# Performance work log

Hardware: AMD Instinct MI355X
Metric: run time of the kernel (lower is better)

The kernel has to match this reference:

```python
import jax, jax.numpy as jnp
import numpy as np

DIM = 2048
NUM_HEADS = 16
HEAD_DIM = DIM // NUM_HEADS
ROPE_BASE = 10000.0


def _rope_cache(seq_len):
    inv_freq = 1.0 / (ROPE_BASE ** (jnp.arange(0, HEAD_DIM, 2, dtype=jnp.float32) / HEAD_DIM))
    t = jnp.arange(seq_len, dtype=jnp.float32)
    freqs = jnp.einsum('i,j->ij', t, inv_freq)          # [S, HEAD_DIM//2]
    emb = jnp.concatenate([freqs, freqs], axis=-1)       # [S, HEAD_DIM]
    return jnp.cos(emb), jnp.sin(emb)


def _rotate_half(x):
    x1, x2 = jnp.split(x, 2, axis=-1)
    return jnp.concatenate([-x2, x1], axis=-1)


def setup_inputs() -> dict:
    key = jax.random.key(0)
    kx, kq, ko = jax.random.split(key, 3)
    B, S = 2, 2048
    x = jax.random.normal(kx, (B, S, DIM), dtype=jnp.float32)
    # torch nn.Linear(dim, 3*dim) weight has shape [3*dim, dim]; y = x @ W.T
    w_qkv = jax.random.normal(kq, (3 * DIM, DIM), dtype=jnp.float32) * (DIM ** -0.5)
    w_out = jax.random.normal(ko, (DIM, DIM), dtype=jnp.float32) * (DIM ** -0.5)
    return {"x": x, "w_qkv": w_qkv, "w_out": w_out}


def reference(x, w_qkv, w_out):
    B, S, _ = x.shape
    qkv = x @ w_qkv.T                                   # [B, S, 3*DIM]
    q, k, v = jnp.split(qkv, 3, axis=-1)
    def to_heads(t):
        return t.reshape(B, S, NUM_HEADS, HEAD_DIM).transpose(0, 2, 1, 3)  # [B, H, S, d]
    q, k, v = to_heads(q), to_heads(k), to_heads(v)

    cos, sin = _rope_cache(S)                           # [S, d]
    cos = cos[None, None, :, :]
    sin = sin[None, None, :, :]
    q = q * cos + _rotate_half(q) * sin
    k = k * cos + _rotate_half(k) * sin

    scale = HEAD_DIM ** -0.5
    scores = jnp.einsum('bhqd,bhkd->bhqk', q, k) * scale  # [B, H, S, S]
    causal = jnp.tril(jnp.ones((S, S), dtype=bool))
    scores = jnp.where(causal[None, None], scores, -jnp.inf)
    attn = jax.nn.softmax(scores, axis=-1)
    out = jnp.einsum('bhqk,bhkd->bhqd', attn, v)          # [B, H, S, d]
    out = out.transpose(0, 2, 1, 3).reshape(B, S, DIM)
    return out @ w_out.T
```

## Files before the change

kernel.cpp:

```cpp
#include <hip/hip_runtime.h>
#include <cstdint>
#include <cstddef>

#define NHEADS 16
#define HDIM   128
#define BATCH  2
#define SEQ    2048
#define DMODEL 2048
#define MTOT   (BATCH*SEQ)
#define NQKV   (3*DMODEL)

typedef __attribute__((ext_vector_type(8))) __bf16 bf16x8;
typedef __attribute__((ext_vector_type(4))) float f32x4;
typedef __attribute__((ext_vector_type(8))) unsigned short ushort8v;

__device__ __forceinline__ unsigned short f2bf(float f){
  __bf16 h = (__bf16)f;
  return __builtin_bit_cast(unsigned short, h);
}
__device__ __forceinline__ float bf2f(unsigned short s){
  return __uint_as_float(((uint32_t)s) << 16);
}
__device__ __forceinline__ void gload_lds16(const void* src, void* lds_base){
  __builtin_amdgcn_global_load_lds((const __attribute__((address_space(1))) unsigned int*)src,
                                   (__attribute__((address_space(3))) unsigned int*)lds_base,
                                   16, 0, 0);
}

template<int CTRL>
__device__ __forceinline__ float dppmv(float x){
  return __uint_as_float((unsigned)__builtin_amdgcn_update_dpp(
      0, (int)__float_as_uint(x), CTRL, 0xF, 0xF, true));
}
__device__ __forceinline__ float rmax16(float x){
  x = fmaxf(x, dppmv<0x128>(x));
  x = fmaxf(x, dppmv<0x124>(x));
  x = fmaxf(x, dppmv<0x122>(x));
  x = fmaxf(x, dppmv<0x121>(x));
  return x;
}
__device__ __forceinline__ float rsum16(float x){
  x += dppmv<0x128>(x);
  x += dppmv<0x124>(x);
  x += dppmv<0x122>(x);
  x += dppmv<0x121>(x);
  return x;
}

__global__ void cast3_kernel(const float* __restrict__ s0, unsigned short* __restrict__ d0, int n0,
                             const float* __restrict__ s1, unsigned short* __restrict__ d1, int n1,
                             const float* __restrict__ s2, unsigned short* __restrict__ d2, int n2){
  const int stride = gridDim.x*blockDim.x*8;
  const int base = (blockIdx.x*blockDim.x + threadIdx.x)*8;
  #pragma unroll 1
  for (int a = 0; a < 3; ++a){
    const float* s = a==0 ? s0 : (a==1 ? s1 : s2);
    unsigned short* d = a==0 ? d0 : (a==1 ? d1 : d2);
    const int n = a==0 ? n0 : (a==1 ? n1 : n2);
    for (int i = base; i < n; i += stride){
      float4 x = *reinterpret_cast<const float4*>(s + i);
      float4 y = *reinterpret_cast<const float4*>(s + i + 4);
      ushort8v o;
      o[0]=f2bf(x.x); o[1]=f2bf(x.y); o[2]=f2bf(x.z); o[3]=f2bf(x.w);
      o[4]=f2bf(y.x); o[5]=f2bf(y.y); o[6]=f2bf(y.z); o[7]=f2bf(y.w);
      *reinterpret_cast<ushort8v*>(d + i) = o;
    }
  }
}

template<int MODE>
__global__ __launch_bounds__(512, 2) void gemm2(
    const unsigned short* __restrict__ A,
    const unsigned short* __restrict__ Bw,
    float* __restrict__ Cf,
    unsigned short* __restrict__ qo,
    unsigned short* __restrict__ ko,
    unsigned short* __restrict__ vo,
    int M, int N, int K)
{
  __shared__ __align__(16) unsigned short smem[49152];
  auto lds = reinterpret_cast<unsigned short (*)[3][128*64]>(smem);

  const int lane = threadIdx.x & 63;
  const int wid  = threadIdx.x >> 6;
  const int wm = wid >> 2, wn = wid & 3;
  const int hi = lane >> 4;
  const int l15 = lane & 15;

  const int nwg = gridDim.x * gridDim.y;
  const int bid = blockIdx.y * gridDim.x + blockIdx.x;
  const int swz = (bid & 7) * (nwg >> 3) + (bid >> 3);
  const int by = swz & 31;
  const int bx = swz >> 5;
  const int m0 = by * 128;
  const int n0 = bx * 256;

  const int NT = K >> 6;

  auto stage = [&](const unsigned short* base, int row0, int k0, int buf, int slot){
    const int rlo = wid << 4;
    #pragma unroll
    for (int i=0;i<2;++i){
      const int r = rlo + i*8 + (lane>>3);
      const int csrc = ((lane&7) ^ (lane>>3)) << 3;
      gload_lds16(base + (size_t)(row0 + r)*K + k0 + csrc,
                  &lds[buf][slot][(rlo + i*8)*64]);
    }
  };
  auto frag = [&](const unsigned short* h, int r, int s){
    return *reinterpret_cast<const bf16x8*>(h + r*64 + ((s ^ (r&7)) << 3));
  };

  f32x4 acc[4][4];
  #pragma unroll
  for (int i=0;i<4;++i)
    #pragma unroll
    for (int j=0;j<4;++j) acc[i][j] = (f32x4){0.f,0.f,0.f,0.f};

  stage(A,  m0,      0, 0, 0);
  stage(Bw, n0,      0, 0, 1);
  stage(Bw, n0+128,  0, 0, 2);
  if (NT > 1){
    stage(A, m0, 64, 1, 0);
    asm volatile("s_waitcnt vmcnt(2)" ::: "memory");
  } else {
    asm volatile("s_waitcnt vmcnt(0)" ::: "memory");
  }
  __builtin_amdgcn_sched_barrier(0);
  __builtin_amdgcn_s_barrier();

  bf16x8 Ar[4][2];
  bf16x8 Br[2][2];

  auto tile_body = [&](int kt, int cur){
    const int nxt = cur ^ 1;
    const unsigned short* Ah = &lds[cur][0][0];
    const unsigned short* Bh = &lds[cur][1 + (wn>>1)][0];
    const int rbase = (wn & 1) * 64;

    #pragma unroll
    for (int fm=0;fm<4;++fm)
      #pragma unroll
      for (int kk=0;kk<2;++kk)
        Ar[fm][kk] = frag(Ah, wm*64 + fm*16 + l15, kk*4 + hi);
    #pragma unroll
    for (int nf=0;nf<2;++nf)
      #pragma unroll
      for (int kk=0;kk<2;++kk)
        Br[nf][kk] = frag(Bh, rbase + nf*16 + l15, kk*4 + hi);
    if (kt+1 < NT){
      stage(Bw, n0,     (kt+1)*64, nxt, 1);
      stage(Bw, n0+128, (kt+1)*64, nxt, 2);
    }
    asm volatile("s_waitcnt lgkmcnt(8)" ::: "memory");
    __builtin_amdgcn_sched_barrier(0);
    __builtin_amdgcn_s_barrier();
    asm volatile("s_waitcnt lgkmcnt(0)" ::: "memory");
    __builtin_amdgcn_sched_barrier(0);
    __builtin_amdgcn_s_setprio(1);
    #pragma unroll
    for (int fm=0;fm<4;++fm){
      acc[fm][0] = __builtin_amdgcn_mfma_f32_16x16x32_bf16(Ar[fm][0], Br[0][0], acc[fm][0], 0,0,0);
      acc[fm][0] = __builtin_amdgcn_mfma_f32_16x16x32_bf16(Ar[fm][1], Br[0][1], acc[fm][0], 0,0,0);
      acc[fm][1] = __builtin_amdgcn_mfma_f32_16x16x32_bf16(Ar[fm][0], Br[1][0], acc[fm][1], 0,0,0);
      acc[fm][1] = __builtin_amdgcn_mfma_f32_16x16x32_bf16(Ar[fm][1], Br[1][1], acc[fm][1], 0,0,0);
    }
    __builtin_amdgcn_s_setprio(0);
    __builtin_amdgcn_sched_barrier(0);
    __builtin_amdgcn_s_barrier();

    #pragma unroll
    for (int nf=0;nf<2;++nf)
      #pragma unroll
      for (int kk=0;kk<2;++kk)
        Br[nf][kk] = frag(Bh, rbase + 32 + nf*16 + l15, kk*4 + hi);
    if (kt+2 < NT) stage(A, m0, (kt+2)*64, cur, 0);
    __builtin_amdgcn_sched_barrier(0);
    __builtin_amdgcn_s_barrier();
    asm volatile("s_waitcnt lgkmcnt(0)" ::: "memory");
    __builtin_amdgcn_sched_barrier(0);
    __builtin_amdgcn_s_setprio(1);
    #pragma unroll
    for (int fm=0;fm<4;++fm){
      acc[fm][2] = __builtin_amdgcn_mfma_f32_16x16x32_bf16(Ar[fm][0], Br[0][0], acc[fm][2], 0,0,0);
      acc[fm][2] = __builtin_amdgcn_mfma_f32_16x16x32_bf16(Ar[fm][1], Br[0][1], acc[fm][2], 0,0,0);
      acc[fm][3] = __builtin_amdgcn_mfma_f32_16x16x32_bf16(Ar[fm][0], Br[1][0], acc[fm][3], 0,0,0);
      acc[fm][3] = __builtin_amdgcn_mfma_f32_16x16x32_bf16(Ar[fm][1], Br[1][1], acc[fm][3], 0,0,0);
    }
    __builtin_amdgcn_s_setprio(0);
    if (kt+2 < NT)      asm volatile("s_waitcnt vmcnt(2)" ::: "memory");
    else if (kt+1 < NT) asm volatile("s_waitcnt vmcnt(0)" ::: "memory");
    __builtin_amdgcn_sched_barrier(0);
    __builtin_amdgcn_s_barrier();
  };

  for (int kt2 = 0; kt2 < NT; kt2 += 2){
    tile_body(kt2,     0);
    tile_body(kt2 + 1, 1);
  }

  if (MODE == 0 && (n0 >> 11) == 2){
    __builtin_amdgcn_s_barrier();
    unsigned short* trsp = smem;
    #pragma unroll
    for (int fm=0;fm<4;++fm){
      const int srow = wm*64 + fm*16 + hi*4;
      #pragma unroll
      for (int p=0;p<4;++p){
        const int dcol = wn*64 + p*16 + l15;
        f32x4 v = acc[fm][p];
        ushort4 pk;
        pk.x=f2bf(v[0]); pk.y=f2bf(v[1]); pk.z=f2bf(v[2]); pk.w=f2bf(v[3]);
        *reinterpret_cast<ushort4*>(trsp + dcol*136 + srow) = pk;
      }
    }
    __syncthreads();
    const int bb  = m0 >> 11;
    const int ss0 = m0 & 2047;
    const size_t vrow = (size_t)(bb*2048 + (n0 - 4096));
    const int t = threadIdx.x;
    #pragma unroll
    for (int it=0; it<8; ++it){
      const int dl = it*32 + (t>>4);
      const int ch = t & 15;
      ushort8v val = *reinterpret_cast<const ushort8v*>(trsp + dl*136 + ch*8);
      *reinterpret_cast<ushort8v*>(vo + (vrow + dl)*SEQ + ss0 + ch*8) = val;
    }
  } else {
    #pragma unroll
    for (int fm=0;fm<4;++fm){
      const int row0 = m0 + wm*64 + fm*16 + (hi<<2);
      #pragma unroll
      for (int p=0;p<4;++p){
        const int col = n0 + wn*64 + p*16 + l15;
        f32x4 v = acc[fm][p];
        if (MODE == 1){
          #pragma unroll
          for (int r=0;r<4;++r) Cf[(size_t)(row0+r)*N + col] = v[r];
        } else {
          const int part = col >> 11;
          const int hh = (col >> 7) & 15;
          const int d  = col & 127;
          const int bb = row0 >> 11;
          const int ss = row0 & 2047;
          unsigned short* base = (part == 0 ? qo : ko)
                               + ((size_t)(bb*NHEADS+hh)*SEQ + ss)*HDIM + d;
          #pragma unroll
          for (int r=0;r<4;++r) base[r*HDIM] = f2bf(v[r]);
        }
      }
    }
  }
}

__global__ __launch_bounds__(256, 2) void gemm_op(
    const unsigned short* __restrict__ A,
    const unsigned short* __restrict__ Bw,
    float* __restrict__ Cf,
    int M, int N, int K)
{
  __shared__ __align__(16) unsigned short smem[2][2][128*64];
  const int lane = threadIdx.x & 63;
  const int wid  = threadIdx.x >> 6;
  const int wm = wid >> 1, wn = wid & 1;
  const int hi = lane >> 4;
  const int l15 = lane & 15;

  const int nwg = gridDim.x * gridDim.y;
  const int bid = blockIdx.y * gridDim.x + blockIdx.x;
  const int swz = (bid & 7) * (nwg >> 3) + (bid >> 3);
  const int by = swz & 31;
  const int bx = swz >> 5;
  const int m0 = by * 128;
  const int n0 = bx * 128;

  const int NT = K >> 6;

  auto stage = [&](const unsigned short* base, int row0, int k0, int buf, int slot){
    const int rlo = wid << 5;
    #pragma unroll
    for (int i=0;i<4;++i){
      const int r = rlo + i*8 + (lane>>3);
      const int csrc = ((lane&7) ^ (lane>>3)) << 3;
      gload_lds16(base + (size_t)(row0 + r)*K + k0 + csrc,
                  &smem[buf][slot][(rlo + i*8)*64]);
    }
  };
  auto frag = [&](const unsigned short* h, int r, int s){
    return *reinterpret_cast<const bf16x8*>(h + r*64 + ((s ^ (r&7)) << 3));
  };

  f32x4 acc[4][4];
  #pragma unroll
  for (int i=0;i<4;++i)
    #pragma unroll
    for (int j=0;j<4;++j) acc[i][j] = (f32x4){0.f,0.f,0.f,0.f};

  stage(A,  m0, 0, 0, 0);
  stage(Bw, n0, 0, 0, 1);
  if (NT > 1){
    stage(A, m0, 64, 1, 0);
    asm volatile("s_waitcnt vmcnt(4)" ::: "memory");
  } else {
    asm volatile("s_waitcnt vmcnt(0)" ::: "memory");
  }
  __builtin_amdgcn_sched_barrier(0);
  __builtin_amdgcn_s_barrier();

  bf16x8 Ar[4][2];
  bf16x8 Br[2][2];

  auto tile_body = [&](int kt, int cur){
    const int nxt = cur ^ 1;
    const unsigned short* Ah = &smem[cur][0][0];
    const unsigned short* Bh = &smem[cur][1][0];
    const int rbase = wn * 64;

    #pragma unroll
    for (int fm=0;fm<4;++fm)
      #pragma unroll
      for (int kk=0;kk<2;++kk)
        Ar[fm][kk] = frag(Ah, wm*64 + fm*16 + l15, kk*4 + hi);
    #pragma unroll
    for (int nf=0;nf<2;++nf)
      #pragma unroll
      for (int kk=0;kk<2;++kk)
        Br[nf][kk] = frag(Bh, rbase + nf*16 + l15, kk*4 + hi);
    if (kt+1 < NT) stage(Bw, n0, (kt+1)*64, nxt, 1);
    asm volatile("s_waitcnt lgkmcnt(8)" ::: "memory");
    __builtin_amdgcn_sched_barrier(0);
    __builtin_amdgcn_s_barrier();
    asm volatile("s_waitcnt lgkmcnt(0)" ::: "memory");
    __builtin_amdgcn_sched_barrier(0);
    __builtin_amdgcn_s_setprio(1);
    #pragma unroll
    for (int fm=0;fm<4;++fm){
      acc[fm][0] = __builtin_amdgcn_mfma_f32_16x16x32_bf16(Ar[fm][0], Br[0][0], acc[fm][0], 0,0,0);
      acc[fm][0] = __builtin_amdgcn_mfma_f32_16x16x32_bf16(Ar[fm][1], Br[0][1], acc[fm][0], 0,0,0);
      acc[fm][1] = __builtin_amdgcn_mfma_f32_16x16x32_bf16(Ar[fm][0], Br[1][0], acc[fm][1], 0,0,0);
      acc[fm][1] = __builtin_amdgcn_mfma_f32_16x16x32_bf16(Ar[fm][1], Br[1][1], acc[fm][1], 0,0,0);
    }
    __builtin_amdgcn_s_setprio(0);
    __builtin_amdgcn_sched_barrier(0);
    __builtin_amdgcn_s_barrier();

    #pragma unroll
    for (int nf=0;nf<2;++nf)
      #pragma unroll
      for (int kk=0;kk<2;++kk)
        Br[nf][kk] = frag(Bh, rbase + 32 + nf*16 + l15, kk*4 + hi);
    if (kt+2 < NT) stage(A, m0, (kt+2)*64, cur, 0);
    __builtin_amdgcn_sched_barrier(0);
    __builtin_amdgcn_s_barrier();
    asm volatile("s_waitcnt lgkmcnt(0)" ::: "memory");
    __builtin_amdgcn_sched_barrier(0);
    __builtin_amdgcn_s_setprio(1);
    #pragma unroll
    for (int fm=0;fm<4;++fm){
      acc[fm][2] = __builtin_amdgcn_mfma_f32_16x16x32_bf16(Ar[fm][0], Br[0][0], acc[fm][2], 0,0,0);
      acc[fm][2] = __builtin_amdgcn_mfma_f32_16x16x32_bf16(Ar[fm][1], Br[0][1], acc[fm][2], 0,0,0);
      acc[fm][3] = __builtin_amdgcn_mfma_f32_16x16x32_bf16(Ar[fm][0], Br[1][0], acc[fm][3], 0,0,0);
      acc[fm][3] = __builtin_amdgcn_mfma_f32_16x16x32_bf16(Ar[fm][1], Br[1][1], acc[fm][3], 0,0,0);
    }
    __builtin_amdgcn_s_setprio(0);
    if (kt+2 < NT)      asm volatile("s_waitcnt vmcnt(4)" ::: "memory");
    else if (kt+1 < NT) asm volatile("s_waitcnt vmcnt(0)" ::: "memory");
    __builtin_amdgcn_sched_barrier(0);
    __builtin_amdgcn_s_barrier();
  };

  for (int kt2 = 0; kt2 < NT; kt2 += 2){
    tile_body(kt2,     0);
    tile_body(kt2 + 1, 1);
  }

  #pragma unroll
  for (int fm=0;fm<4;++fm){
    const int row0 = m0 + wm*64 + fm*16 + (hi<<2);
    #pragma unroll
    for (int p=0;p<4;++p){
      const int col = n0 + wn*64 + p*16 + l15;
      f32x4 v = acc[fm][p];
      #pragma unroll
      for (int r=0;r<4;++r) Cf[(size_t)(row0+r)*N + col] = v[r];
    }
  }
}

__global__ void rope_kernel(unsigned short* __restrict__ qh, unsigned short* __restrict__ kh){
  const int idx = blockIdx.x * blockDim.x + threadIdx.x;
  const int j  = idx & 63;
  const int s  = (idx >> 6) & 2047;
  const int bh = (idx >> 17) & 31;
  const int t  = idx >> 22;
  unsigned short* base = (t ? kh : qh) + ((size_t)bh*SEQ + s)*HDIM;
  const float x1 = bf2f(base[j]);
  const float x2 = bf2f(base[j+64]);
  const float inv = exp2f(-(float)j * (13.287712379549449f/64.f));
  const float ang = (float)s * inv;
  float sn, cs;
  sincosf(ang, &sn, &cs);
  float o1 = x1*cs - x2*sn;
  float o2 = x2*cs + x1*sn;
  const float QSCALE = 0.08838834764831845f * 1.4426950408889634f;
  if (t == 0){ o1 *= QSCALE; o2 *= QSCALE; }
  base[j]    = f2bf(o1);
  base[j+64] = f2bf(o2);
}

__global__ __launch_bounds__(256, 2) void attn_kernel(
    const unsigned short* __restrict__ qh,
    const unsigned short* __restrict__ kh,
    const unsigned short* __restrict__ vT,
    unsigned short* __restrict__ ao)
{
  __shared__ __align__(16) unsigned short Ks[2][64*128];
  __shared__ __align__(16) unsigned short Vs[2][128*64];
  __shared__ __align__(16) unsigned short Ps[4][16*64];

  const int lane = threadIdx.x & 63;
  const int wid  = threadIdx.x >> 6;
  const int hi   = lane >> 4;
  const int l15  = lane & 15;
  const int pr = blockIdx.x;
  const int bh = blockIdx.y;
  const int b_ = bh >> 4, h_ = bh & 15;

  const unsigned short* Qb = qh + (size_t)bh * SEQ * HDIM;
  const unsigned short* Kb = kh + (size_t)bh * SEQ * HDIM;
  const unsigned short* Vb = vT + (size_t)bh * HDIM * SEQ;

  const int qrowf[2] = { pr*64 + wid*16, (31-pr)*64 + wid*16 };

  auto stageKV = [&](int kg, int buf){
    #pragma unroll
    for (int i=0;i<4;++i){
      const int r  = (wid*4+i)*4 + (lane>>4);
      const int cb = ((lane&15)<<4) ^ ((r&7)<<4);
      gload_lds16(Kb + (size_t)(kg*64 + r)*HDIM + (cb>>1), &Ks[buf][0] + (wid*4+i)*512);
    }
    #pragma unroll
    for (int i=0;i<4;++i){
      const int d  = (wid*4+i)*8 + (lane>>3);
      const int cb = ((lane&7)<<4) ^ ((d&7)<<4);
      gload_lds16(Vb + (size_t)d*SEQ + kg*64 + (cb>>1), &Vs[buf][0] + (wid*4+i)*512);
    }
  };

  bf16x8 qf[2][4];
  #pragma unroll
  for (int fi=0; fi<2; ++fi){
    const int qr = qrowf[fi] + l15;
    #pragma unroll
    for (int ks = 0; ks < 4; ++ks)
      qf[fi][ks] = *reinterpret_cast<const bf16x8*>(Qb + (size_t)qr*HDIM + ks*32 + hi*8);
  }

  f32x4 oacc[2][8];
  #pragma unroll
  for (int fi=0;fi<2;++fi)
    #pragma unroll
    for (int t=0;t<8;++t) oacc[fi][t] = (f32x4){0.f,0.f,0.f,0.f};
  float mrun[2][4], lrun[2][4];
  #pragma unroll
  for (int fi=0;fi<2;++fi)
    #pragma unroll
    for (int r=0;r<4;++r){ mrun[fi][r] = -3.0e38f; lrun[fi][r] = 0.f; }

  const int nkt = 32 - pr;

  stageKV(0, 0);
  __syncthreads();

  for (int kt = 0; kt < nkt; ++kt){
    const int cur = kt & 1;
    if (kt + 1 < nkt) stageKV(kt + 1, cur ^ 1);

    const bool lo_act = (kt <= pr);

    f32x4 sacc[2][4];
    #pragma unroll
    for (int fi=0;fi<2;++fi)
      #pragma unroll
      for (int nt=0;nt<4;++nt) sacc[fi][nt] = (f32x4){0.f,0.f,0.f,0.f};
    __builtin_amdgcn_s_setprio(1);
    #pragma unroll
    for (int nt=0;nt<4;++nt){
      const int krow = nt*16 + l15;
      bf16x8 kf[4];
      #pragma unroll
      for (int ks=0;ks<4;++ks){
        const int cb = (ks*64 + (hi<<4)) ^ ((krow&7)<<4);
        kf[ks] = *reinterpret_cast<const bf16x8*>(&Ks[cur][0] + krow*128 + (cb>>1));
      }
      #pragma unroll
      for (int ks=0;ks<4;++ks)
        sacc[1][nt] = __builtin_amdgcn_mfma_f32_16x16x32_bf16(qf[1][ks], kf[ks], sacc[1][nt], 0,0,0);
      if (lo_act){
        #pragma unroll
        for (int ks=0;ks<4;++ks)
          sacc[0][nt] = __builtin_amdgcn_mfma_f32_16x16x32_bf16(qf[0][ks], kf[ks], sacc[0][nt], 0,0,0);
      }
    }
    __builtin_amdgcn_s_setprio(0);

    char* pb = (char*)&Ps[wid][0];
    #pragma unroll
    for (int fi=0; fi<2; ++fi){
      if (fi == 0 && !lo_act) continue;

      if (kt*64 + 63 > qrowf[fi]){
        #pragma unroll
        for (int nt=0;nt<4;++nt){
          const int key = kt*64 + nt*16 + l15;
          #pragma unroll
          for (int r=0;r<4;++r){
            const int qr = qrowf[fi] + hi*4 + r;
            if (key > qr) sacc[fi][nt][r] = -1.0e30f;
          }
        }
      }

      float mx[4]; float need = 0.f;
      #pragma unroll
      for (int r=0;r<4;++r){
        float m_ = fmaxf(fmaxf(sacc[fi][0][r], sacc[fi][1][r]),
                         fmaxf(sacc[fi][2][r], sacc[fi][3][r]));
        m_ = rmax16(m_);
        mx[r] = m_;
        need = fmaxf(need, m_ - mrun[fi][r]);
      }
      if (!__all(need <= 8.0f)){
        float fac[4];
        #pragma unroll
        for (int r=0;r<4;++r){
          const float mnew = fmaxf(mrun[fi][r], mx[r]);
          fac[r] = exp2f(mrun[fi][r] - mnew);
          mrun[fi][r] = mnew;
          lrun[fi][r] *= fac[r];
        }
        #pragma unroll
        for (int t=0;t<8;++t)
          #pragma unroll
          for (int r=0;r<4;++r) oacc[fi][t][r] *= fac[r];
      }
      #pragma unroll
      for (int r=0;r<4;++r){
        float ps = 0.f;
        #pragma unroll
        for (int nt=0;nt<4;++nt){
          const float p = exp2f(sacc[fi][nt][r] - mrun[fi][r]);
          sacc[fi][nt][r] = p;
          ps += p;
        }
        ps = rsum16(ps);
        lrun[fi][r] += ps;
      }

      #pragma unroll
      for (int nt=0;nt<4;++nt){
        const int keyb = (nt*16 + l15) << 1;
        #pragma unroll
        for (int r=0;r<4;++r){
          const int prow = hi*4 + r;
          *(unsigned short*)(pb + prow*128 + (keyb ^ ((prow&7)<<4))) = f2bf(sacc[fi][nt][r]);
        }
      }
      asm volatile("s_waitcnt lgkmcnt(0)" ::: "memory");
      __builtin_amdgcn_sched_barrier(0);

      bf16x8 pa[2];
      {
        const int prow = l15;
        #pragma unroll
        for (int ks=0;ks<2;++ks){
          const int pcb = (ks*64 + (hi<<4)) ^ ((prow&7)<<4);
          pa[ks] = *reinterpret_cast<const bf16x8*>(pb + prow*128 + pcb);
        }
      }
      __builtin_amdgcn_s_setprio(1);
      #pragma unroll
      for (int ks=0;ks<2;++ks){
        #pragma unroll
        for (int t=0;t<8;++t){
          const int drow = t*16 + l15;
          const int vcb = (ks*64 + (hi<<4)) ^ ((drow&7)<<4);
          bf16x8 vb = *reinterpret_cast<const bf16x8*>(&Vs[cur][0] + drow*64 + (vcb>>1));
          oacc[fi][t] = __builtin_amdgcn_mfma_f32_16x16x32_bf16(pa[ks], vb, oacc[fi][t], 0,0,0);
        }
      }
      __builtin_amdgcn_s_setprio(0);
    }

    __syncthreads();
  }

  #pragma unroll
  for (int fi=0;fi<2;++fi){
    float linv[4];
    #pragma unroll
    for (int r=0;r<4;++r) linv[r] = 1.0f / lrun[fi][r];
    #pragma unroll
    for (int t=0;t<8;++t){
      const int col = h_*HDIM + t*16 + l15;
      #pragma unroll
      for (int r=0;r<4;++r){
        const int s_ = qrowf[fi] + hi*4 + r;
        ao[(size_t)(b_*SEQ + s_)*DMODEL + col] = f2bf(oacc[fi][t][r] * linv[r]);
      }
    }
  }
}

extern "C" void kernel_launch(void* const* d_in, const int* in_sizes, int n_in,
                              void* d_out, int out_size, void* d_ws, size_t ws_size,
                              hipStream_t stream)
{
  const float* x     = (const float*)d_in[0];
  const float* w_qkv = (const float*)d_in[1];
  const float* w_out = (const float*)d_in[2];
  float* out = (float*)d_out;

  unsigned short* xb    = (unsigned short*)d_ws;
  unsigned short* wqkvb = xb    + (size_t)MTOT*DMODEL;
  unsigned short* woutb = wqkvb + (size_t)NQKV*DMODEL;
  unsigned short* qhb   = woutb + (size_t)DMODEL*DMODEL;
  unsigned short* khb   = qhb   + (size_t)MTOT*DMODEL;
  unsigned short* vtb   = khb   + (size_t)MTOT*DMODEL;
  unsigned short* aob   = vtb   + (size_t)MTOT*DMODEL;

  hipLaunchKernelGGL(cast3_kernel, dim3(1024), dim3(256), 0, stream,
                     x, xb, MTOT*DMODEL, w_qkv, wqkvb, NQKV*DMODEL, w_out, woutb, DMODEL*DMODEL);
  hipLaunchKernelGGL((gemm2<0>), dim3(NQKV/256, MTOT/128), dim3(512), 0, stream,
                     xb, wqkvb, (float*)nullptr, qhb, khb, vtb, MTOT, NQKV, DMODEL);
  hipLaunchKernelGGL(rope_kernel, dim3((2*BATCH*NHEADS*SEQ*64)/256), dim3(256), 0, stream, qhb, khb);
  hipLaunchKernelGGL(attn_kernel, dim3(16, BATCH*NHEADS), dim3(256), 0, stream, qhb, khb, vtb, aob);
  hipLaunchKernelGGL(gemm_op, dim3(DMODEL/128, MTOT/128), dim3(256), 0, stream,
                     aob, woutb, out, MTOT, DMODEL, DMODEL);
}
```

Measured before the change: 262.3 us.

## Fuse RoPE and Q scaling into QKV GEMM epilogue via LDS staging

```diff
diff --git a/kernel.cpp b/kernel.cpp
--- a/kernel.cpp
+++ b/kernel.cpp
@@ -200,7 +200,6 @@
   }
 
   if (MODE == 0 && (n0 >> 11) == 2){
-    __builtin_amdgcn_s_barrier();
     unsigned short* trsp = smem;
     #pragma unroll
     for (int fm=0;fm<4;++fm){
@@ -226,6 +225,52 @@
       ushort8v val = *reinterpret_cast<const ushort8v*>(trsp + dl*136 + ch*8);
       *reinterpret_cast<ushort8v*>(vo + (vrow + dl)*SEQ + ss0 + ch*8) = val;
     }
+  } else if (MODE == 0){
+    unsigned short* trsp = smem;
+    #pragma unroll
+    for (int fm=0;fm<4;++fm){
+      const int rowl = wm*64 + fm*16 + hi*4;
+      #pragma unroll
+      for (int p=0;p<4;++p){
+        const int c = wn*64 + p*16 + l15;
+        f32x4 v = acc[fm][p];
+        #pragma unroll
+        for (int r=0;r<4;++r) trsp[(rowl+r)*264 + c] = f2bf(v[r]);
+      }
+    }
+    __syncthreads();
+    const bool isq = (n0 >> 11) == 0;
+    unsigned short* dst = isq ? qo : ko;
+    const float QS = 0.08838834764831845f * 1.4426950408889634f;
+    const int t = threadIdx.x;
+    #pragma unroll
+    for (int it=0; it<4; ++it){
+      const int v = it*512 + t;
+      const int rv = v >> 4;
+      const int head = (v >> 3) & 1;
+      const int jb = (v & 7) * 8;
+      ushort8v a = *reinterpret_cast<const ushort8v*>(trsp + rv*264 + head*128 + jb);
+      ushort8v b = *reinterpret_cast<const ushort8v*>(trsp + rv*264 + head*128 + 64 + jb);
+      const int grow = m0 + rv;
+      const int ss = grow & 2047, bb = grow >> 11;
+      const int hh = ((n0 >> 7) & 15) + head;
+      ushort8v o1, o2;
+      #pragma unroll
+      for (int e=0;e<8;++e){
+        const int j = jb + e;
+        const float inv = exp2f(-(float)j * (13.287712379549449f/64.f));
+        float sn, cs;
+        sincosf((float)ss * inv, &sn, &cs);
+        float x1 = bf2f(a[e]), x2 = bf2f(b[e]);
+        float r1 = x1*cs - x2*sn;
+        float r2 = x2*cs + x1*sn;
+        if (isq){ r1 *= QS; r2 *= QS; }
+        o1[e] = f2bf(r1); o2[e] = f2bf(r2);
+      }
+      unsigned short* base = dst + ((size_t)(bb*NHEADS+hh)*SEQ + ss)*HDIM;
+      *reinterpret_cast<ushort8v*>(base + jb)      = o1;
+      *reinterpret_cast<ushort8v*>(base + 64 + jb) = o2;
+    }
   } else {
     #pragma unroll
     for (int fm=0;fm<4;++fm){
@@ -234,20 +279,8 @@
       for (int p=0;p<4;++p){
         const int col = n0 + wn*64 + p*16 + l15;
         f32x4 v = acc[fm][p];
-        if (MODE == 1){
-          #pragma unroll
-          for (int r=0;r<4;++r) Cf[(size_t)(row0+r)*N + col] = v[r];
-        } else {
-          const int part = col >> 11;
-          const int hh = (col >> 7) & 15;
-          const int d  = col & 127;
-          const int bb = row0 >> 11;
-          const int ss = row0 & 2047;
-          unsigned short* base = (part == 0 ? qo : ko)
-                               + ((size_t)(bb*NHEADS+hh)*SEQ + ss)*HDIM + d;
-          #pragma unroll
-          for (int r=0;r<4;++r) base[r*HDIM] = f2bf(v[r]);
-        }
+        #pragma unroll
+        for (int r=0;r<4;++r) Cf[(size_t)(row0+r)*N + col] = v[r];
       }
     }
   }
@@ -387,27 +420,6 @@
   }
 }
 
-__global__ void rope_kernel(unsigned short* __restrict__ qh, unsigned short* __restrict__ kh){
-  const int idx = blockIdx.x * blockDim.x + threadIdx.x;
-  const int j  = idx & 63;
-  const int s  = (idx >> 6) & 2047;
-  const int bh = (idx >> 17) & 31;
-  const int t  = idx >> 22;
-  unsigned short* base = (t ? kh : qh) + ((size_t)bh*SEQ + s)*HDIM;
-  const float x1 = bf2f(base[j]);
-  const float x2 = bf2f(base[j+64]);
-  const float inv = exp2f(-(float)j * (13.287712379549449f/64.f));
-  const float ang = (float)s * inv;
-  float sn, cs;
-  sincosf(ang, &sn, &cs);
-  float o1 = x1*cs - x2*sn;
-  float o2 = x2*cs + x1*sn;
-  const float QSCALE = 0.08838834764831845f * 1.4426950408889634f;
-  if (t == 0){ o1 *= QSCALE; o2 *= QSCALE; }
-  base[j]    = f2bf(o1);
-  base[j+64] = f2bf(o2);
-}
-
 __global__ __launch_bounds__(256, 2) void attn_kernel(
     const unsigned short* __restrict__ qh,
     const unsigned short* __restrict__ kh,
@@ -633,7 +645,6 @@
                      x, xb, MTOT*DMODEL, w_qkv, wqkvb, NQKV*DMODEL, w_out, woutb, DMODEL*DMODEL);
   hipLaunchKernelGGL((gemm2<0>), dim3(NQKV/256, MTOT/128), dim3(512), 0, stream,
                      xb, wqkvb, (float*)nullptr, qhb, khb, vtb, MTOT, NQKV, DMODEL);
-  hipLaunchKernelGGL(rope_kernel, dim3((2*BATCH*NHEADS*SEQ*64)/256), dim3(256), 0, stream, qhb, khb);
   hipLaunchKernelGGL(attn_kernel, dim3(16, BATCH*NHEADS), dim3(256), 0, stream, qhb, khb, vtb, aob);
   hipLaunchKernelGGL(gemm_op, dim3(DMODEL/128, MTOT/128), dim3(256), 0, stream,
                      aob, woutb, out, MTOT, DMODEL, DMODEL);
```

New measurement: 259.1 us. About the same (-1.2%).
